# Optimization experiments

Hardware: AMD Instinct MI355X
Metric: run time of the kernel (lower is better)

The kernel has to match this reference:

```python
import jax, jax.numpy as jnp
import numpy as np

NODE_DIM = 256
OUTPUT_DIM = 256
NUM_HOPS = 4
NUM_NODES = 25000
NUM_EDGES = 400000
NUM_TYPES = 10
FEAT_DIM = 32


def setup_inputs() -> dict:
    key = jax.random.key(0)
    ks = jax.random.split(key, 12)
    nodes = jax.random.normal(ks[0], (NUM_NODES, FEAT_DIM), dtype=jnp.float32)
    edges = jax.random.randint(ks[1], (2, NUM_EDGES), 0, NUM_NODES, dtype=jnp.int64)
    node_types = jax.random.randint(ks[2], (NUM_NODES,), 0, NUM_TYPES, dtype=jnp.int64)
    s = 0.02
    type_emb = jax.random.normal(ks[3], (NUM_TYPES, NODE_DIM), dtype=jnp.float32) * s
    W_proj = jax.random.normal(ks[4], (FEAT_DIM, NODE_DIM), dtype=jnp.float32) * s
    b_proj = jnp.zeros((NODE_DIM,), dtype=jnp.float32)
    W_msg = jax.random.normal(ks[5], (NUM_HOPS, 2 * NODE_DIM, NODE_DIM), dtype=jnp.float32) * s
    b_msg = jnp.zeros((NUM_HOPS, NODE_DIM), dtype=jnp.float32)
    W_upd = jax.random.normal(ks[6], (NUM_HOPS, 2 * NODE_DIM, NODE_DIM), dtype=jnp.float32) * s
    b_upd = jnp.zeros((NUM_HOPS, NODE_DIM), dtype=jnp.float32)
    W_out = jax.random.normal(ks[7], (NODE_DIM, OUTPUT_DIM), dtype=jnp.float32) * s
    b_out = jnp.zeros((OUTPUT_DIM,), dtype=jnp.float32)
    return {"nodes": nodes, "edges": edges, "node_types": node_types,
            "type_emb": type_emb, "W_proj": W_proj, "b_proj": b_proj,
            "W_msg": W_msg, "b_msg": b_msg, "W_upd": W_upd, "b_upd": b_upd,
            "W_out": W_out, "b_out": b_out}


def reference(nodes, edges, node_types, type_emb, W_proj, b_proj,
              W_msg, b_msg, W_upd, b_upd, W_out, b_out):
    n = nodes.shape[0]
    src, dst = edges[0], edges[1]
    # initial node states: linear proj + type embedding
    h = nodes @ W_proj + b_proj + type_emb[node_types]  # [N, D]
    for i in range(NUM_HOPS):
        edge_feat = jnp.concatenate([h[src], h[dst]], axis=1)      # [E, 2D]
        messages = edge_feat @ W_msg[i] + b_msg[i]                 # [E, D]
        agg = jax.ops.segment_sum(messages, dst, num_segments=n)   # [N, D]
        h = jax.nn.relu(jnp.concatenate([h, agg], axis=1) @ W_upd[i] + b_upd[i])
    graph_embedding = jnp.max(h, axis=0)                           # [D]
    return graph_embedding @ W_out + b_out                          # [output_dim]
```

## Files before the change

kernel.cpp:

```cpp
#include <hip/hip_runtime.h>
#include <hip/hip_bf16.h>

#define NDIM 256
#define FDIM 32
#define HOPS 4
#define NPB 16

typedef __attribute__((ext_vector_type(8))) short short8;
typedef __attribute__((ext_vector_type(4))) float f32x4;
typedef __attribute__((ext_vector_type(2))) float f32x2;

__device__ inline float b2f(unsigned short u) {
    union { unsigned int i; float f; } v; v.i = ((unsigned int)u) << 16; return v.f;
}
__device__ inline unsigned short f2b(float f) {
    union { float f; unsigned int i; } v; v.f = f;
    unsigned int r = v.i + 0x7FFF + ((v.i >> 16) & 1);
    return (unsigned short)(r >> 16);
}
__device__ inline unsigned char f2fp8(float v) {
    return (unsigned char)(__builtin_amdgcn_cvt_pk_fp8_f32(v, v, 0, false) & 0xFF);
}

__global__ __launch_bounds__(256) void prep_mega_kernel(
        const int* __restrict__ dst, int* __restrict__ deg, int E, int histB,
        const float* __restrict__ Wm, const float* __restrict__ Wu,
        const float* __restrict__ bm,
        unsigned short* __restrict__ WtB,
        unsigned short* __restrict__ Am, unsigned short* __restrict__ BmT,
        float* __restrict__ cvec, int* __restrict__ geInt,
        unsigned char* __restrict__ h8row,
        const float* __restrict__ nodes, const int* __restrict__ node_types,
        const float* __restrict__ type_emb, const float* __restrict__ W_proj,
        const float* __restrict__ b_proj,
        unsigned short* __restrict__ h, unsigned char* __restrict__ h8, int n) {
    __shared__ float T[32][33];
    __shared__ float sb[512];
    int b = blockIdx.x;
    int t = threadIdx.x;

    if (b < histB) {
        int e = (b * 256 + t) * 4;
        if (e + 3 < E) {
            int4 d = *(const int4*)(dst + e);
            atomicAdd(&deg[d.x], 1);
            atomicAdd(&deg[d.y], 1);
            atomicAdd(&deg[d.z], 1);
            atomicAdd(&deg[d.w], 1);
        } else {
            for (int k = e; k < E; ++k) atomicAdd(&deg[dst[k]], 1);
        }
    } else if (b < histB + 773) {
        int bb = b - histB;
        if (bb < 256) {
            int hop = bb >> 6;
            int rem = bb & 63;
            int k0 = (rem & 7) * 32, n0 = (rem >> 3) * 32;
            const float* src = Wu + (size_t)hop * 512 * 256;
            unsigned short* dstp = WtB + (size_t)hop * 256 * 256;
            int tr = t >> 5, tc = t & 31;
#pragma unroll
            for (int r = 0; r < 4; ++r) {
                int k = tr + r * 8;
                T[tc][k] = src[(size_t)(k0 + k) * 256 + n0 + tc];
            }
            __syncthreads();
#pragma unroll
            for (int r = 0; r < 4; ++r) {
                int nn = tr + r * 8;
                dstp[(size_t)(n0 + nn) * 256 + k0 + tc] = f2b(T[nn][tc]);
            }
        } else if (bb < 260) {
            int hop = bb - 256;
            sb[t] = bm[hop * 256 + t];
            __syncthreads();
            const float* B = Wu + (size_t)hop * 512 * 256 + (size_t)256 * 256;
            float acc = 0.f;
#pragma unroll 8
            for (int j = 0; j < 256; ++j) acc += sb[j] * B[(size_t)j * 256 + t];
            cvec[hop * 256 + t] = acc;
        } else if (bb == 260) {
            geInt[t] = 0;
            h8row[t] = 0;
        } else if (bb < 517) {
            size_t base = (size_t)(bb - 261) * 2048 + (size_t)t * 8;
            float4 a0 = *(const float4*)(Wm + base);
            float4 a1 = *(const float4*)(Wm + base + 4);
            ushort4 o0, o1;
            o0.x = f2b(a0.x); o0.y = f2b(a0.y); o0.z = f2b(a0.z); o0.w = f2b(a0.w);
            o1.x = f2b(a1.x); o1.y = f2b(a1.y); o1.z = f2b(a1.z); o1.w = f2b(a1.w);
            *(ushort4*)(Am + base) = o0;
            *(ushort4*)(Am + base + 4) = o1;
        } else {
            int tb = bb - 517;
            int hop = tb >> 6;
            int rem = tb & 63;
            int j0 = (rem & 7) * 32, n0 = (rem >> 3) * 32;
            const float* srcp = Wu + (size_t)hop * 512 * 256 + (size_t)256 * 256;
            unsigned short* dstp = BmT + (size_t)hop * 256 * 256;
            int tr = t >> 5, tc = t & 31;
#pragma unroll
            for (int r = 0; r < 4; ++r) {
                int j = tr + r * 8;
                T[tc][j] = srcp[(size_t)(j0 + j) * 256 + n0 + tc];
            }
            __syncthreads();
#pragma unroll
            for (int r = 0; r < 4; ++r) {
                int nn = tr + r * 8;
                dstp[(size_t)(n0 + nn) * 256 + j0 + tc] = f2b(T[nn][tc]);
            }
        }
    } else {
        int v0 = (b - histB - 773) * NPB;
#pragma unroll
        for (int s = 0; s < 2; ++s) {
            int idx = t + s * 256;
            int j = idx >> 5, f = idx & 31;
            int v = v0 + j;
            sb[idx] = (v < n) ? nodes[(size_t)v * FDIM + f] : 0.f;
        }
        __syncthreads();
        float acc[NPB];
#pragma unroll
        for (int j = 0; j < NPB; ++j) {
            int v = v0 + j;
            acc[j] = (v < n) ? (b_proj[t] + type_emb[(size_t)node_types[v] * NDIM + t]) : 0.f;
        }
#pragma unroll 4
        for (int k = 0; k < FDIM; ++k) {
            float wv = W_proj[(size_t)k * NDIM + t];
#pragma unroll
            for (int j = 0; j < NPB; ++j)
                acc[j] += sb[j * FDIM + k] * wv;
        }
#pragma unroll
        for (int j = 0; j < NPB; ++j) {
            int v = v0 + j;
            if (v < n) {
                h[(size_t)v * NDIM + t] = f2b(acc[j]);
                h8[(size_t)v * NDIM + t] = f2fp8(acc[j]);
            }
        }
    }
}

__global__ __launch_bounds__(1024) void scan1_mm_kernel(
        const int* __restrict__ deg, int* __restrict__ rowptr,
        int* __restrict__ bsum, int nch, int n,
        const unsigned short* __restrict__ Am, const unsigned short* __restrict__ BmT,
        unsigned short* __restrict__ WtA, unsigned short* __restrict__ WtC) {
    int t = threadIdx.x;
    int b = blockIdx.x;
    if (b < nch) {
        __shared__ int wsum[16];
        int i = b * 1024 + t;
        int v = 0;
        if (i < n) v = (deg[i] + 7) & ~7;
        int lane = t & 63, wid = t >> 6;
        int x = v;
#pragma unroll
        for (int d = 1; d < 64; d <<= 1) {
            int u = __shfl_up(x, d, 64);
            if (lane >= d) x += u;
        }
        if (lane == 63) wsum[wid] = x;
        __syncthreads();
        if (wid == 0) {
            int ws = (lane < 16) ? wsum[lane] : 0;
#pragma unroll
            for (int d = 1; d < 16; d <<= 1) {
                int u = __shfl_up(ws, d, 64);
                if (lane >= d) ws += u;
            }
            if (lane < 16) wsum[lane] = ws;
        }
        __syncthreads();
        int excl = (wid > 0 ? wsum[wid - 1] : 0) + x - v;
        if (i < n) rowptr[i] = excl;
        if (t == 1023) bsum[b] = wsum[15];
        return;
    }

    int m = b - nch;
    int hop = m >> 1, which = m & 1;
    const unsigned short* A = Am + (size_t)m * 65536;
    const unsigned short* B = BmT + (size_t)hop * 65536;
    unsigned short* W = (which ? WtC : WtA) + (size_t)hop * 65536;
    int wave = t >> 6, lane = t & 63;
    int l16 = lane & 15, quad = lane >> 4;
    int k0 = (wave & 3) * 64;
    int n0 = (wave >> 2) * 64;
    f32x4 acc[4][4];
#pragma unroll
    for (int i = 0; i < 4; ++i)
#pragma unroll
        for (int j = 0; j < 4; ++j) acc[i][j] = (f32x4)(0.f);

    for (int j0 = 0; j0 < 256; j0 += 32) {
        short8 af[4], bfr[4];
#pragma unroll
        for (int kt = 0; kt < 4; ++kt)
            af[kt] = *(const short8*)(A + (size_t)(k0 + kt * 16 + l16) * 256 + j0 + quad * 8);
#pragma unroll
        for (int nt = 0; nt < 4; ++nt)
            bfr[nt] = *(const short8*)(B + (size_t)(n0 + nt * 16 + l16) * 256 + j0 + quad * 8);
#pragma unroll
        for (int kt = 0; kt < 4; ++kt)
#pragma unroll
            for (int nt = 0; nt < 4; ++nt)
                acc[kt][nt] = __builtin_amdgcn_mfma_f32_16x16x32_bf16(af[kt], bfr[nt], acc[kt][nt], 0, 0, 0);
    }
#pragma unroll
    for (int kt = 0; kt < 4; ++kt)
#pragma unroll
        for (int nt = 0; nt < 4; ++nt) {
            int k = k0 + kt * 16 + quad * 4;
            int nn = n0 + nt * 16 + l16;
            ushort4 o;
            o.x = f2b(acc[kt][nt][0]); o.y = f2b(acc[kt][nt][1]);
            o.z = f2b(acc[kt][nt][2]); o.w = f2b(acc[kt][nt][3]);
            *(ushort4*)&W[(size_t)nn * 256 + k] = o;
        }
}

__global__ __launch_bounds__(1024) void scan2_kernel(
        int* __restrict__ rowptr, int* __restrict__ cursor,
        const int* __restrict__ bsum, int nch, int n) {
    __shared__ int soff, stot;
    int t = threadIdx.x;
    int b = blockIdx.x;
    if (t < 64) {
        int s = (t < nch) ? bsum[t] : 0;
        int x = s;
#pragma unroll
        for (int d = 1; d < 64; d <<= 1) {
            int u = __shfl_up(x, d, 64);
            if (t >= d) x += u;
        }
        if (t == 63) stot = x;
        if (t == b) soff = x - s;
    }
    __syncthreads();
    int i = b * 1024 + t;
    if (i < n) {
        int r = rowptr[i] + soff;
        rowptr[i] = r;
        cursor[i] = r;
    }
    if (b == 0 && t == 0) rowptr[n] = stot;
}

__global__ void fillpad_kernel(const int* __restrict__ src, const int* __restrict__ dst,
                               int* __restrict__ cursor,
                               const int* __restrict__ rowptr, const int* __restrict__ deg,
                               int* __restrict__ col, int E, int fillB, int n) {
    int b = blockIdx.x;
    int t = threadIdx.x;
    if (b < fillB) {
        int e = b * 256 + t;
        if (e < E) {
            int d = dst[e];
            int p = atomicAdd(&cursor[d], 1);
            col[p] = src[e];
        }
    } else {
        int v = (b - fillB) * 256 + t;
        if (v < n) {
            int s = rowptr[v] + deg[v];
            int e0 = rowptr[v + 1];
            for (int i = s; i < e0; ++i) col[i] = n;
        }
    }
}

__global__ __launch_bounds__(256) void agg_kernel(const unsigned char* __restrict__ h8,
                                                  const int* __restrict__ rowptr,
                                                  const int* __restrict__ col,
                                                  unsigned short* __restrict__ S, int n) {
    int wave = threadIdx.x >> 6;
    int lane = threadIdx.x & 63;
    int half = lane >> 5;
    int hl = lane & 31;
    int v = blockIdx.x * 8 + wave * 2 + half;
    if (v >= n) return;
    int beg = rowptr[v], end = rowptr[v + 1];
    float a[8];
#pragma unroll
    for (int e = 0; e < 8; ++e) a[e] = 0.f;
    int cofs = hl * 8;
    int i = beg;
    if (i + 16 <= end) {
        int4 cA0 = *(const int4*)(col + i);
        int4 cA1 = *(const int4*)(col + i + 4);
        int4 cA2 = *(const int4*)(col + i + 8);
        int4 cA3 = *(const int4*)(col + i + 12);
        for (; i + 32 <= end; i += 16) {
            int4 cB0 = *(const int4*)(col + i + 16);
            int4 cB1 = *(const int4*)(col + i + 20);
            int4 cB2 = *(const int4*)(col + i + 24);
            int4 cB3 = *(const int4*)(col + i + 28);
            int4 c4[4] = {cA0, cA1, cA2, cA3};
            const int* cc = (const int*)c4;
            uint2 x[16];
#pragma unroll
            for (int j = 0; j < 16; ++j)
                x[j] = *(const uint2*)(h8 + (size_t)cc[j] * NDIM + cofs);
#pragma unroll
            for (int j = 0; j < 16; ++j) {
                f32x2 p0 = __builtin_amdgcn_cvt_pk_f32_fp8(x[j].x, false);
                f32x2 p1 = __builtin_amdgcn_cvt_pk_f32_fp8(x[j].x, true);
                f32x2 p2 = __builtin_amdgcn_cvt_pk_f32_fp8(x[j].y, false);
                f32x2 p3 = __builtin_amdgcn_cvt_pk_f32_fp8(x[j].y, true);
                a[0] += p0[0]; a[1] += p0[1]; a[2] += p1[0]; a[3] += p1[1];
                a[4] += p2[0]; a[5] += p2[1]; a[6] += p3[0]; a[7] += p3[1];
            }
            cA0 = cB0; cA1 = cB1; cA2 = cB2; cA3 = cB3;
        }
        {
            int4 c4[4] = {cA0, cA1, cA2, cA3};
            const int* cc = (const int*)c4;
            uint2 x[16];
#pragma unroll
            for (int j = 0; j < 16; ++j)
                x[j] = *(const uint2*)(h8 + (size_t)cc[j] * NDIM + cofs);
#pragma unroll
            for (int j = 0; j < 16; ++j) {
                f32x2 p0 = __builtin_amdgcn_cvt_pk_f32_fp8(x[j].x, false);
                f32x2 p1 = __builtin_amdgcn_cvt_pk_f32_fp8(x[j].x, true);
                f32x2 p2 = __builtin_amdgcn_cvt_pk_f32_fp8(x[j].y, false);
                f32x2 p3 = __builtin_amdgcn_cvt_pk_f32_fp8(x[j].y, true);
                a[0] += p0[0]; a[1] += p0[1]; a[2] += p1[0]; a[3] += p1[1];
                a[4] += p2[0]; a[5] += p2[1]; a[6] += p3[0]; a[7] += p3[1];
            }
            i += 16;
        }
    }
    for (; i < end; i += 8) {
        int4 c4[2];
        c4[0] = *(const int4*)(col + i);
        c4[1] = *(const int4*)(col + i + 4);
        const int* cc = (const int*)c4;
        uint2 x[8];
#pragma unroll
        for (int j = 0; j < 8; ++j)
            x[j] = *(const uint2*)(h8 + (size_t)cc[j] * NDIM + cofs);
#pragma unroll
        for (int j = 0; j < 8; ++j) {
            f32x2 p0 = __builtin_amdgcn_cvt_pk_f32_fp8(x[j].x, false);
            f32x2 p1 = __builtin_amdgcn_cvt_pk_f32_fp8(x[j].x, true);
            f32x2 p2 = __builtin_amdgcn_cvt_pk_f32_fp8(x[j].y, false);
            f32x2 p3 = __builtin_amdgcn_cvt_pk_f32_fp8(x[j].y, true);
            a[0] += p0[0]; a[1] += p0[1]; a[2] += p1[0]; a[3] += p1[1];
            a[4] += p2[0]; a[5] += p2[1]; a[6] += p3[0]; a[7] += p3[1];
        }
    }
    uint4 o;
    unsigned short* op = (unsigned short*)&o;
#pragma unroll
    for (int e = 0; e < 8; ++e) op[e] = f2b(a[e]);
    *(uint4*)&S[(size_t)v * NDIM + cofs] = o;
}

#define BM 128
#define BN 64
#define BK 64

template <bool LAST>
__global__ __launch_bounds__(256, 4) void gemm_hop_kernel(const unsigned short* __restrict__ S,
                                                          const unsigned short* __restrict__ hcur,
                                                          const int* __restrict__ deg,
                                                          const unsigned short* __restrict__ WtA,
                                                          const unsigned short* __restrict__ WtB,
                                                          const unsigned short* __restrict__ WtC,
                                                          const float* __restrict__ bupd,
                                                          const float* __restrict__ cvec,
                                                          unsigned short* __restrict__ Out,
                                                          unsigned char* __restrict__ Out8,
                                                          int* __restrict__ geInt, int n) {
    __shared__ unsigned short As[BM * BK];
    __shared__ unsigned short Bs[BN * BK];
    __shared__ unsigned short Cs[BN * BK];
    __shared__ int smax[BN];

    int gx = (n + BM - 1) / BM;
    int bid = blockIdx.x;
    int xcd = bid & 7;
    int q = bid >> 3;
    int g = (q >> 2) * 8 + xcd;
    int by = q & 3;
    if (g >= gx) return;
    int row0 = g * BM;
    int n0 = by * BN;

    int t = threadIdx.x;
    int lane = t & 63;
    int w = t >> 6;
    int wm = w >> 1, wn = w & 1;
    int quad = lane >> 4, l16 = lane & 15;

    if (LAST) {
        if (t < BN) smax[t] = 0;
    }

    f32x4 acc1[4][2], acc2[4][2];
#pragma unroll
    for (int i = 0; i < 4; ++i)
#pragma unroll
        for (int j = 0; j < 2; ++j) { acc1[i][j] = (f32x4)(0.f); acc2[i][j] = (f32x4)(0.f); }

    for (int k0 = 0; k0 < NDIM; k0 += BK) {
        __syncthreads();
#pragma unroll
        for (int h2 = 0; h2 < 4; ++h2) {
            int c = t + h2 * 256;
            int r = c >> 3;
            int cb = (c & 7) ^ (r & 7);
            int grow = row0 + r; if (grow >= n) grow = n - 1;
            __builtin_amdgcn_global_load_lds(
                (const unsigned int*)(S + (size_t)grow * NDIM + k0 + cb * 8),
                (unsigned int*)(As + (size_t)(h2 * 256 + w * 64) * 8), 16, 0, 0);
        }
#pragma unroll
        for (int h2 = 0; h2 < 2; ++h2) {
            int c = t + h2 * 256;
            int r = c >> 3;
            int cb = (c & 7) ^ (r & 7);
            __builtin_amdgcn_global_load_lds(
                (const unsigned int*)(WtA + (size_t)(n0 + r) * NDIM + k0 + cb * 8),
                (unsigned int*)(Bs + (size_t)(h2 * 256 + w * 64) * 8), 16, 0, 0);
        }
        __syncthreads();
#pragma unroll
        for (int ks = 0; ks < BK; ks += 32) {
            short8 af[4], bf[2];
#pragma unroll
            for (int mt = 0; mt < 4; ++mt) {
                int ar = wm * 64 + mt * 16 + l16;
                int acb = ((ks >> 3) + quad) ^ (ar & 7);
                af[mt] = *(const short8*)&As[ar * BK + acb * 8];
            }
#pragma unroll
            for (int nt = 0; nt < 2; ++nt) {
                int br = wn * 32 + nt * 16 + l16;
                int bcb = ((ks >> 3) + quad) ^ (br & 7);
                bf[nt] = *(const short8*)&Bs[br * BK + bcb * 8];
            }
#pragma unroll
            for (int mt = 0; mt < 4; ++mt)
#pragma unroll
                for (int nt = 0; nt < 2; ++nt)
                    acc1[mt][nt] = __builtin_amdgcn_mfma_f32_16x16x32_bf16(af[mt], bf[nt], acc1[mt][nt], 0, 0, 0);
        }
    }
    for (int k0 = 0; k0 < NDIM; k0 += BK) {
        __syncthreads();
#pragma unroll
        for (int h2 = 0; h2 < 4; ++h2) {
            int c = t + h2 * 256;
            int r = c >> 3;
            int cb = (c & 7) ^ (r & 7);
            int grow = row0 + r; if (grow >= n) grow = n - 1;
            __builtin_amdgcn_global_load_lds(
                (const unsigned int*)(hcur + (size_t)grow * NDIM + k0 + cb * 8),
                (unsigned int*)(As + (size_t)(h2 * 256 + w * 64) * 8), 16, 0, 0);
        }
#pragma unroll
        for (int h2 = 0; h2 < 2; ++h2) {
            int c = t + h2 * 256;
            int r = c >> 3;
            int cb = (c & 7) ^ (r & 7);
            size_t widx = (size_t)(n0 + r) * NDIM + k0 + cb * 8;
            __builtin_amdgcn_global_load_lds(
                (const unsigned int*)(WtB + widx),
                (unsigned int*)(Bs + (size_t)(h2 * 256 + w * 64) * 8), 16, 0, 0);
            __builtin_amdgcn_global_load_lds(
                (const unsigned int*)(WtC + widx),
                (unsigned int*)(Cs + (size_t)(h2 * 256 + w * 64) * 8), 16, 0, 0);
        }
        __syncthreads();
#pragma unroll
        for (int ks = 0; ks < BK; ks += 32) {
            short8 af[4], bf[2], cf[2];
#pragma unroll
            for (int mt = 0; mt < 4; ++mt) {
                int ar = wm * 64 + mt * 16 + l16;
                int acb = ((ks >> 3) + quad) ^ (ar & 7);
                af[mt] = *(const short8*)&As[ar * BK + acb * 8];
            }
#pragma unroll
            for (int nt = 0; nt < 2; ++nt) {
                int br = wn * 32 + nt * 16 + l16;
                int bcb = ((ks >> 3) + quad) ^ (br & 7);
                bf[nt] = *(const short8*)&Bs[br * BK + bcb * 8];
                cf[nt] = *(const short8*)&Cs[br * BK + bcb * 8];
            }
#pragma unroll
            for (int mt = 0; mt < 4; ++mt)
#pragma unroll
                for (int nt = 0; nt < 2; ++nt) {
                    acc1[mt][nt] = __builtin_amdgcn_mfma_f32_16x16x32_bf16(af[mt], bf[nt], acc1[mt][nt], 0, 0, 0);
                    acc2[mt][nt] = __builtin_amdgcn_mfma_f32_16x16x32_bf16(af[mt], cf[nt], acc2[mt][nt], 0, 0, 0);
                }
        }
    }
#pragma unroll
    for (int mt = 0; mt < 4; ++mt) {
#pragma unroll
        for (int nt = 0; nt < 2; ++nt) {
            int lcol = wn * 32 + nt * 16 + l16;
            int col = n0 + lcol;
            float bu = bupd[col];
            float cv = cvec[col];
            float cmax = 0.f;
#pragma unroll
            for (int r = 0; r < 4; ++r) {
                int row = row0 + wm * 64 + mt * 16 + quad * 4 + r;
                if (row < n) {
                    float dg = (float)deg[row];
                    float v = fmaxf(acc1[mt][nt][r] + dg * (acc2[mt][nt][r] + cv) + bu, 0.f);
                    Out[(size_t)row * NDIM + col] = f2b(v);
                    if (!LAST) Out8[(size_t)row * NDIM + col] = f2fp8(v);
                    if (LAST) cmax = fmaxf(cmax, v);
                }
            }
            if (LAST) atomicMax(&smax[lcol], __float_as_int(cmax));
        }
    }
    if (LAST) {
        __syncthreads();
        if (t < BN) atomicMax(&geInt[n0 + t], smax[t]);
    }
}

__global__ __launch_bounds__(1024) void out_kernel(const float* __restrict__ ge,
                                                   const float* __restrict__ W_out,
                                                   const float* __restrict__ b_out,
                                                   float* __restrict__ out) {
    __shared__ float red[4][NDIM];
    int t = threadIdx.x & 255;
    int g = threadIdx.x >> 8;
    float acc = 0.f;
#pragma unroll 8
    for (int kk = 0; kk < 64; ++kk) {
        int k = g * 64 + kk;
        acc += ge[k] * W_out[k * NDIM + t];
    }
    red[g][t] = acc;
    __syncthreads();
    if (g == 0)
        out[t] = b_out[t] + red[0][t] + red[1][t] + red[2][t] + red[3][t];
}

extern "C" void kernel_launch(void* const* d_in, const int* in_sizes, int n_in,
                              void* d_out, int out_size, void* d_ws, size_t ws_size,
                              hipStream_t stream) {
    const float* nodes      = (const float*)d_in[0];
    const int*   edges      = (const int*)d_in[1];
    const int*   node_types = (const int*)d_in[2];
    const float* type_emb   = (const float*)d_in[3];
    const float* W_proj     = (const float*)d_in[4];
    const float* b_proj     = (const float*)d_in[5];
    const float* W_msg      = (const float*)d_in[6];
    const float* b_msg      = (const float*)d_in[7];
    const float* W_upd      = (const float*)d_in[8];
    const float* b_upd      = (const float*)d_in[9];
    const float* W_out      = (const float*)d_in[10];
    const float* b_out      = (const float*)d_in[11];

    int n = in_sizes[2];
    int E = in_sizes[1] / 2;
    const int* src = edges;
    const int* dst = edges + E;

    size_t off = 0;
    auto alloc = [&](size_t bytes) {
        void* p = (char*)d_ws + off;
        off += (bytes + 255) & ~(size_t)255;
        return p;
    };
    int* deg    = (int*)alloc((size_t)(n + 4096) * 4);
    int* rowptr = (int*)alloc((size_t)(n + 1) * 4);
    int* cursor = (int*)alloc((size_t)n * 4);
    int* bsum   = (int*)alloc((size_t)256 * 4);
    int* col    = (int*)alloc((size_t)(E + 8 * n) * 4);
    unsigned short* WtA = (unsigned short*)alloc((size_t)HOPS * 256 * 256 * 2);
    unsigned short* WtB = (unsigned short*)alloc((size_t)HOPS * 256 * 256 * 2);
    unsigned short* WtC = (unsigned short*)alloc((size_t)HOPS * 256 * 256 * 2);
    unsigned short* Am  = (unsigned short*)alloc((size_t)8 * 256 * 256 * 2);
    unsigned short* BmT = (unsigned short*)alloc((size_t)HOPS * 256 * 256 * 2);
    float* cvec = (float*)alloc((size_t)HOPS * 256 * 4);
    int* geInt  = (int*)alloc((size_t)256 * 4);
    unsigned short* hA  = (unsigned short*)alloc((size_t)(n + 1) * NDIM * 2);
    unsigned short* hB  = (unsigned short*)alloc((size_t)(n + 1) * NDIM * 2);
    unsigned short* Sb  = (unsigned short*)alloc((size_t)n * NDIM * 2);
    unsigned char* h8   = (unsigned char*)alloc((size_t)(n + 1) * NDIM);

    hipMemsetAsync(deg, 0, (size_t)(n + 4096) * 4, stream);
    int hb = (E + 1023) / 1024;
    int eb = (E + 255) / 256;
    int pb = (n + 255) / 256;
    int ib = (n + NPB - 1) / NPB;
    int nch = (n + 1023) / 1024;
    prep_mega_kernel<<<hb + 773 + ib, 256, 0, stream>>>(
        dst, deg, E, hb,
        W_msg, W_upd, b_msg, WtB, Am, BmT, cvec, geInt, h8 + (size_t)n * NDIM,
        nodes, node_types, type_emb, W_proj, b_proj, hA, h8, n);
    scan1_mm_kernel<<<nch + 8, 1024, 0, stream>>>(deg, rowptr, bsum, nch, n, Am, BmT, WtA, WtC);
    scan2_kernel<<<nch, 1024, 0, stream>>>(rowptr, cursor, bsum, nch, n);
    fillpad_kernel<<<eb + pb, 256, 0, stream>>>(src, dst, cursor, rowptr, deg, col, E, eb, n);

    unsigned short* h  = hA;
    unsigned short* ho = hB;
    int gx = (n + BM - 1) / BM;
    int ggrid = 8 * ((gx + 7) / 8) * 4;
    for (int i = 0; i < HOPS; ++i) {
        agg_kernel<<<(n + 7) / 8, 256, 0, stream>>>(h8, rowptr, col, Sb, n);
        size_t wofs = (size_t)i * 256 * 256;
        if (i == HOPS - 1)
            gemm_hop_kernel<true><<<ggrid, 256, 0, stream>>>(
                Sb, h, deg, WtA + wofs, WtB + wofs, WtC + wofs,
                b_upd + (size_t)i * NDIM, cvec + (size_t)i * NDIM, ho, h8, geInt, n);
        else
            gemm_hop_kernel<false><<<ggrid, 256, 0, stream>>>(
                Sb, h, deg, WtA + wofs, WtB + wofs, WtC + wofs,
                b_upd + (size_t)i * NDIM, cvec + (size_t)i * NDIM, ho, h8, geInt, n);
        unsigned short* tmp = h; h = ho; ho = tmp;
    }
    out_kernel<<<1, 1024, 0, stream>>>((const float*)geInt, W_out, b_out, (float*)d_out);
}
```

Before: 328.5 us.

## Fuse output projection into last GEMM, vectorize CSR fill and agg accumulators

Removes the separate out_kernel launch. The last GEMM block to finish, detected through an atomic done counter, now computes the final W_out projection. The last hop also stops writing h to global memory, since only the column max is needed. fillpad now processes four edges per thread using int4 loads, and agg_kernel accumulates into packed float2 vectors so the compiler can use packed adds. The main risk is in the last-block pattern: it depends on threadfence ordering, and the single finishing block does the whole final matvec serially.

```diff
diff --git a/kernel.cpp b/kernel.cpp
--- a/kernel.cpp
+++ b/kernel.cpp
@@ -28,7 +28,7 @@
         const float* __restrict__ bm,
         unsigned short* __restrict__ WtB,
         unsigned short* __restrict__ Am, unsigned short* __restrict__ BmT,
-        float* __restrict__ cvec, int* __restrict__ geInt,
+        float* __restrict__ cvec, int* __restrict__ geInt, int* __restrict__ done,
         unsigned char* __restrict__ h8row,
         const float* __restrict__ nodes, const int* __restrict__ node_types,
         const float* __restrict__ type_emb, const float* __restrict__ W_proj,
@@ -82,6 +82,7 @@
         } else if (bb == 260) {
             geInt[t] = 0;
             h8row[t] = 0;
+            if (t == 0) *done = 0;
         } else if (bb < 517) {
             size_t base = (size_t)(bb - 261) * 2048 + (size_t)t * 8;
             float4 a0 = *(const float4*)(Wm + base);
@@ -258,11 +259,19 @@
     int b = blockIdx.x;
     int t = threadIdx.x;
     if (b < fillB) {
-        int e = b * 256 + t;
-        if (e < E) {
-            int d = dst[e];
-            int p = atomicAdd(&cursor[d], 1);
-            col[p] = src[e];
+        int e = (b * 256 + t) * 4;
+        if (e + 3 < E) {
+            int4 s4 = *(const int4*)(src + e);
+            int4 d4 = *(const int4*)(dst + e);
+            col[atomicAdd(&cursor[d4.x], 1)] = s4.x;
+            col[atomicAdd(&cursor[d4.y], 1)] = s4.y;
+            col[atomicAdd(&cursor[d4.z], 1)] = s4.z;
+            col[atomicAdd(&cursor[d4.w], 1)] = s4.w;
+        } else {
+            for (int k = e; k < E; ++k) {
+                int d = dst[k];
+                col[atomicAdd(&cursor[d], 1)] = src[k];
+            }
         }
     } else {
         int v = (b - fillB) * 256 + t;
@@ -285,9 +294,7 @@
     int v = blockIdx.x * 8 + wave * 2 + half;
     if (v >= n) return;
     int beg = rowptr[v], end = rowptr[v + 1];
-    float a[8];
-#pragma unroll
-    for (int e = 0; e < 8; ++e) a[e] = 0.f;
+    f32x2 A0 = (f32x2)(0.f), A1 = (f32x2)(0.f), A2 = (f32x2)(0.f), A3 = (f32x2)(0.f);
     int cofs = hl * 8;
     int i = beg;
     if (i + 16 <= end) {
@@ -308,12 +315,10 @@
                 x[j] = *(const uint2*)(h8 + (size_t)cc[j] * NDIM + cofs);
 #pragma unroll
             for (int j = 0; j < 16; ++j) {
-                f32x2 p0 = __builtin_amdgcn_cvt_pk_f32_fp8(x[j].x, false);
-                f32x2 p1 = __builtin_amdgcn_cvt_pk_f32_fp8(x[j].x, true);
-                f32x2 p2 = __builtin_amdgcn_cvt_pk_f32_fp8(x[j].y, false);
-                f32x2 p3 = __builtin_amdgcn_cvt_pk_f32_fp8(x[j].y, true);
-                a[0] += p0[0]; a[1] += p0[1]; a[2] += p1[0]; a[3] += p1[1];
-                a[4] += p2[0]; a[5] += p2[1]; a[6] += p3[0]; a[7] += p3[1];
+                A0 += __builtin_amdgcn_cvt_pk_f32_fp8(x[j].x, false);
+                A1 += __builtin_amdgcn_cvt_pk_f32_fp8(x[j].x, true);
+                A2 += __builtin_amdgcn_cvt_pk_f32_fp8(x[j].y, false);
+                A3 += __builtin_amdgcn_cvt_pk_f32_fp8(x[j].y, true);
             }
             cA0 = cB0; cA1 = cB1; cA2 = cB2; cA3 = cB3;
         }
@@ -326,12 +331,10 @@
                 x[j] = *(const uint2*)(h8 + (size_t)cc[j] * NDIM + cofs);
 #pragma unroll
             for (int j = 0; j < 16; ++j) {
-                f32x2 p0 = __builtin_amdgcn_cvt_pk_f32_fp8(x[j].x, false);
-                f32x2 p1 = __builtin_amdgcn_cvt_pk_f32_fp8(x[j].x, true);
-                f32x2 p2 = __builtin_amdgcn_cvt_pk_f32_fp8(x[j].y, false);
-                f32x2 p3 = __builtin_amdgcn_cvt_pk_f32_fp8(x[j].y, true);
-                a[0] += p0[0]; a[1] += p0[1]; a[2] += p1[0]; a[3] += p1[1];
-                a[4] += p2[0]; a[5] += p2[1]; a[6] += p3[0]; a[7] += p3[1];
+                A0 += __builtin_amdgcn_cvt_pk_f32_fp8(x[j].x, false);
+                A1 += __builtin_amdgcn_cvt_pk_f32_fp8(x[j].x, true);
+                A2 += __builtin_amdgcn_cvt_pk_f32_fp8(x[j].y, false);
+                A3 += __builtin_amdgcn_cvt_pk_f32_fp8(x[j].y, true);
             }
             i += 16;
         }
@@ -347,18 +350,18 @@
             x[j] = *(const uint2*)(h8 + (size_t)cc[j] * NDIM + cofs);
 #pragma unroll
         for (int j = 0; j < 8; ++j) {
-            f32x2 p0 = __builtin_amdgcn_cvt_pk_f32_fp8(x[j].x, false);
-            f32x2 p1 = __builtin_amdgcn_cvt_pk_f32_fp8(x[j].x, true);
-            f32x2 p2 = __builtin_amdgcn_cvt_pk_f32_fp8(x[j].y, false);
-            f32x2 p3 = __builtin_amdgcn_cvt_pk_f32_fp8(x[j].y, true);
-            a[0] += p0[0]; a[1] += p0[1]; a[2] += p1[0]; a[3] += p1[1];
-            a[4] += p2[0]; a[5] += p2[1]; a[6] += p3[0]; a[7] += p3[1];
+            A0 += __builtin_amdgcn_cvt_pk_f32_fp8(x[j].x, false);
+            A1 += __builtin_amdgcn_cvt_pk_f32_fp8(x[j].x, true);
+            A2 += __builtin_amdgcn_cvt_pk_f32_fp8(x[j].y, false);
+            A3 += __builtin_amdgcn_cvt_pk_f32_fp8(x[j].y, true);
         }
     }
     uint4 o;
     unsigned short* op = (unsigned short*)&o;
-#pragma unroll
-    for (int e = 0; e < 8; ++e) op[e] = f2b(a[e]);
+    op[0] = f2b(A0[0]); op[1] = f2b(A0[1]);
+    op[2] = f2b(A1[0]); op[3] = f2b(A1[1]);
+    op[4] = f2b(A2[0]); op[5] = f2b(A2[1]);
+    op[6] = f2b(A3[0]); op[7] = f2b(A3[1]);
     *(uint4*)&S[(size_t)v * NDIM + cofs] = o;
 }
 
@@ -377,7 +380,11 @@
                                                           const float* __restrict__ cvec,
                                                           unsigned short* __restrict__ Out,
                                                           unsigned char* __restrict__ Out8,
-                                                          int* __restrict__ geInt, int n) {
+                                                          int* __restrict__ geInt,
+                                                          int* __restrict__ done, int active,
+                                                          const float* __restrict__ W_out,
+                                                          const float* __restrict__ b_out,
+                                                          float* __restrict__ out, int n) {
     __shared__ unsigned short As[BM * BK];
     __shared__ unsigned short Bs[BN * BK];
     __shared__ unsigned short Cs[BN * BK];
@@ -519,9 +526,12 @@
                 if (row < n) {
                     float dg = (float)deg[row];
                     float v = fmaxf(acc1[mt][nt][r] + dg * (acc2[mt][nt][r] + cv) + bu, 0.f);
-                    Out[(size_t)row * NDIM + col] = f2b(v);
-                    if (!LAST) Out8[(size_t)row * NDIM + col] = f2fp8(v);
-                    if (LAST) cmax = fmaxf(cmax, v);
+                    if (!LAST) {
+                        Out[(size_t)row * NDIM + col] = f2b(v);
+                        Out8[(size_t)row * NDIM + col] = f2fp8(v);
+                    } else {
+                        cmax = fmaxf(cmax, v);
+                    }
                 }
             }
             if (LAST) atomicMax(&smax[lcol], __float_as_int(cmax));
@@ -530,26 +540,23 @@
     if (LAST) {
         __syncthreads();
         if (t < BN) atomicMax(&geInt[n0 + t], smax[t]);
-    }
-}
-
-__global__ __launch_bounds__(1024) void out_kernel(const float* __restrict__ ge,
-                                                   const float* __restrict__ W_out,
-                                                   const float* __restrict__ b_out,
-                                                   float* __restrict__ out) {
-    __shared__ float red[4][NDIM];
-    int t = threadIdx.x & 255;
-    int g = threadIdx.x >> 8;
-    float acc = 0.f;
+        __threadfence();
+        __shared__ int amLast;
+        if (t == 0) amLast = (atomicAdd(done, 1) == active - 1);
+        __syncthreads();
+        if (amLast) {
+            __threadfence();
+            __shared__ float geS[NDIM];
+            int gi = atomicAdd(&geInt[t], 0);
+            geS[t] = __int_as_float(gi);
+            __syncthreads();
+            float acc = b_out[t];
 #pragma unroll 8
-    for (int kk = 0; kk < 64; ++kk) {
-        int k = g * 64 + kk;
-        acc += ge[k] * W_out[k * NDIM + t];
-    }
-    red[g][t] = acc;
-    __syncthreads();
-    if (g == 0)
-        out[t] = b_out[t] + red[0][t] + red[1][t] + red[2][t] + red[3][t];
+            for (int k = 0; k < NDIM; ++k)
+                acc += geS[k] * W_out[(size_t)k * NDIM + t];
+            out[t] = acc;
+        }
+    }
 }
 
 extern "C" void kernel_launch(void* const* d_in, const int* in_sizes, int n_in,
@@ -591,6 +598,7 @@
     unsigned short* BmT = (unsigned short*)alloc((size_t)HOPS * 256 * 256 * 2);
     float* cvec = (float*)alloc((size_t)HOPS * 256 * 4);
     int* geInt  = (int*)alloc((size_t)256 * 4);
+    int* done   = (int*)alloc((size_t)256 * 4);
     unsigned short* hA  = (unsigned short*)alloc((size_t)(n + 1) * NDIM * 2);
     unsigned short* hB  = (unsigned short*)alloc((size_t)(n + 1) * NDIM * 2);
     unsigned short* Sb  = (unsigned short*)alloc((size_t)n * NDIM * 2);
@@ -598,34 +606,36 @@
 
     hipMemsetAsync(deg, 0, (size_t)(n + 4096) * 4, stream);
     int hb = (E + 1023) / 1024;
-    int eb = (E + 255) / 256;
+    int fb = (E + 1023) / 1024;
     int pb = (n + 255) / 256;
     int ib = (n + NPB - 1) / NPB;
     int nch = (n + 1023) / 1024;
     prep_mega_kernel<<<hb + 773 + ib, 256, 0, stream>>>(
         dst, deg, E, hb,
-        W_msg, W_upd, b_msg, WtB, Am, BmT, cvec, geInt, h8 + (size_t)n * NDIM,
+        W_msg, W_upd, b_msg, WtB, Am, BmT, cvec, geInt, done, h8 + (size_t)n * NDIM,
         nodes, node_types, type_emb, W_proj, b_proj, hA, h8, n);
     scan1_mm_kernel<<<nch + 8, 1024, 0, stream>>>(deg, rowptr, bsum, nch, n, Am, BmT, WtA, WtC);
     scan2_kernel<<<nch, 1024, 0, stream>>>(rowptr, cursor, bsum, nch, n);
-    fillpad_kernel<<<eb + pb, 256, 0, stream>>>(src, dst, cursor, rowptr, deg, col, E, eb, n);
+    fillpad_kernel<<<fb + pb, 256, 0, stream>>>(src, dst, cursor, rowptr, deg, col, E, fb, n);
 
     unsigned short* h  = hA;
     unsigned short* ho = hB;
     int gx = (n + BM - 1) / BM;
     int ggrid = 8 * ((gx + 7) / 8) * 4;
+    int active = gx * 4;
     for (int i = 0; i < HOPS; ++i) {
         agg_kernel<<<(n + 7) / 8, 256, 0, stream>>>(h8, rowptr, col, Sb, n);
         size_t wofs = (size_t)i * 256 * 256;
         if (i == HOPS - 1)
             gemm_hop_kernel<true><<<ggrid, 256, 0, stream>>>(
                 Sb, h, deg, WtA + wofs, WtB + wofs, WtC + wofs,
-                b_upd + (size_t)i * NDIM, cvec + (size_t)i * NDIM, ho, h8, geInt, n);
+                b_upd + (size_t)i * NDIM, cvec + (size_t)i * NDIM, ho, h8, geInt,
+                done, active, W_out, b_out, (float*)d_out, n);
         else
             gemm_hop_kernel<false><<<ggrid, 256, 0, stream>>>(
                 Sb, h, deg, WtA + wofs, WtB + wofs, WtC + wofs,
-                b_upd + (size_t)i * NDIM, cvec + (size_t)i * NDIM, ho, h8, geInt, n);
+                b_upd + (size_t)i * NDIM, cvec + (size_t)i * NDIM, ho, h8, geInt,
+                done, active, W_out, b_out, (float*)d_out, n);
         unsigned short* tmp = h; h = ho; ho = tmp;
     }
-    out_kernel<<<1, 1024, 0, stream>>>((const float*)geInt, W_out, b_out, (float*)d_out);
-}
+}
```

After: 374.5 us. +14.0%, slower.
